# Kernel tuning notes

Hardware: AMD Instinct MI355X
Metric: run time of the kernel (lower is better)

The kernel has to match this reference:

```python
import jax, jax.numpy as jnp
import numpy as np

NUM_PER_PATH = 16
MARGIN_INTRA = 0.1
MARGIN_INTER = 1.0


def setup_inputs() -> dict:
    key = jax.random.key(0)
    # [B, block_num, 1, 1, 2]; trailing dims must multiply to 2 (see _get_center view)
    path_fea = jax.random.normal(key, (131072, 64, 1, 1, 2), dtype=jnp.float32)
    return {"path_fea": path_fea}


def reference(path_fea):
    B, block = path_fea.shape[0], path_fea.shape[1]
    D = block * 2                     # flattened per-sample feature dim
    G = B // NUM_PER_PATH             # number of centers (groups)
    fea = path_fea.reshape(B, D)      # [B, D] (matches path_fea[j].view(-1))

    # center: mean over the NUM_PER_PATH samples of each group, per block
    # (identical math to the permute/view dance in _get_center)
    grouped = fea.reshape(G, NUM_PER_PATH, D)          # [G, P, D]
    center = jnp.mean(grouped, axis=1)                 # [G, D]

    # ---- inter loss: hinge on pairwise euclidean distances between centers ----
    sq = jnp.sum(center * center, axis=1)              # [G]
    gram = center @ center.T                           # [G, G]
    d2 = jnp.maximum(sq[:, None] + sq[None, :] - 2.0 * gram, 0.0)
    pair_mask = jnp.triu(jnp.ones((G, G), dtype=bool), k=1)  # i < j
    d = jnp.sqrt(jnp.where(pair_mask, d2, 1.0))        # safe sqrt off-mask
    hinge = jnp.maximum(MARGIN_INTER - d, 0.0) ** 2
    n_pairs = G * (G - 1) / 2.0
    inter_loss = jnp.sum(jnp.where(pair_mask, hinge, 0.0)) / n_pairs

    # ---- intra loss: hinge on distance of each sample to its group center ----
    diff = grouped - center[:, None, :]                # [G, P, D]
    di = jnp.sqrt(jnp.sum(diff * diff, axis=-1))       # [G, P]
    intra_loss = jnp.sum(jnp.maximum(di - MARGIN_INTRA, 0.0) ** 2) / (G * NUM_PER_PATH)

    return (inter_loss, intra_loss)
```

## Files before the change

kernel.cpp:

```cpp
#include <hip/hip_runtime.h>
#include <hip/hip_bf16.h>
#include <math.h>

#define B_ROWS   131072
#define D_DIM    128
#define P_SAMP   16
#define G_GROUPS 8192
#define T128     64
#define NTRI2    2080
#define K1_BLOCKS (G_GROUPS / 4)

typedef __bf16 bf16x8  __attribute__((ext_vector_type(8)));
typedef float  floatx4 __attribute__((ext_vector_type(4)));
typedef unsigned short u16x8 __attribute__((ext_vector_type(8)));


__device__ __forceinline__ float wave_red64(float v) {
    #pragma unroll
    for (int off = 32; off > 0; off >>= 1) v += __shfl_xor(v, off, 64);
    return v;
}

__global__ __launch_bounds__(256) void k_center_intra(
    const float* __restrict__ x,
    uint2* __restrict__ cfrag,
    float* __restrict__ sq,
    float* __restrict__ partial,
    float* __restrict__ acc)
{
    const int wave = threadIdx.x >> 6;
    const int lane = threadIdx.x & 63;
    const int half = lane >> 5;
    const int c    = lane & 31;
    const int g    = blockIdx.x * 4 + wave;

    if (blockIdx.x == 0 && threadIdx.x == 0) acc[0] = 0.f;

    const float* base = x + (size_t)g * (P_SAMP * D_DIM) + half * D_DIM + c * 4;

    floatx4 v[8];
    #pragma unroll
    for (int l = 0; l < 8; ++l)
        v[l] = *(const floatx4*)(base + l * (2 * D_DIM));

    floatx4 cs = v[0];
    #pragma unroll
    for (int l = 1; l < 8; ++l) cs += v[l];
    #pragma unroll
    for (int k = 0; k < 4; ++k) cs[k] += __shfl_xor(cs[k], 32, 64);
    floatx4 ctr = cs * (1.0f / P_SAMP);

    float p[9];
    #pragma unroll
    for (int l = 0; l < 8; ++l) {
        floatx4 d = v[l] - ctr;
        p[l] = d[0]*d[0] + d[1]*d[1] + d[2]*d[2] + d[3]*d[3];
    }
    p[8] = ctr[0]*ctr[0] + ctr[1]*ctr[1] + ctr[2]*ctr[2] + ctr[3]*ctr[3];

    #pragma unroll
    for (int off = 16; off > 0; off >>= 1) {
        #pragma unroll
        for (int s = 0; s < 9; ++s) p[s] += __shfl_xor(p[s], off, 64);
    }

    if (half == 0) {
        unsigned int b0 = __builtin_bit_cast(unsigned short, (__bf16)ctr[0]);
        unsigned int b1 = __builtin_bit_cast(unsigned short, (__bf16)ctr[1]);
        unsigned int b2 = __builtin_bit_cast(unsigned short, (__bf16)ctr[2]);
        unsigned int b3 = __builtin_bit_cast(unsigned short, (__bf16)ctr[3]);
        uint2 pk;
        pk.x = (b1 << 16) | b0;
        pk.y = (b3 << 16) | b2;
        const int gran = (g >> 4) * 256 + (c >> 1) * 16 + (g & 15);
        cfrag[gran * 2 + (c & 1)] = pk;
    }
    if (lane == 0) sq[g] = p[8];

    float isum = 0.f;
    #pragma unroll
    for (int l = 0; l < 8; ++l) {
        float d = sqrtf(p[l]);
        float t = fmaxf(d - 0.1f, 0.f);
        isum += t * t;
    }
    isum += __shfl_xor(isum, 32, 64);

    __shared__ float sh[4];
    if (lane == 0) sh[wave] = isum;
    __syncthreads();
    if (threadIdx.x == 0)
        partial[blockIdx.x] = sh[0] + sh[1] + sh[2] + sh[3];
}

__global__ __launch_bounds__(256) void k_inter(
    const u16x8* __restrict__ cfrag,
    const float* __restrict__ sq,
    float* __restrict__ acc)
{
    __shared__ u16x8 smem[4096];

    const int bid = blockIdx.x;
    float sf = sqrtf(64.5f * 64.5f - 2.0f * (float)bid);
    int ti = (int)(64.5f - sf);
    if (ti < 0) ti = 0;
    if (ti > T128 - 1) ti = T128 - 1;
    #define TRI_OFF(i) ((i) * T128 - (((i) * ((i) - 1)) >> 1))
    while (ti > 0 && TRI_OFF(ti) > bid) --ti;
    while (ti < T128 - 1 && TRI_OFF(ti + 1) <= bid) ++ti;
    const int tj = ti + (bid - TRI_OFF(ti));
    #undef TRI_OFF

    const int t = threadIdx.x;
    const size_t abase = (size_t)ti * 2048;
    const size_t bbase = (size_t)tj * 2048;
    #pragma unroll
    for (int it = 0; it < 8; ++it) {
        const int idx = t + it * 256;
        smem[idx]        = cfrag[abase + idx];
        smem[idx + 2048] = cfrag[bbase + idx];
    }
    __syncthreads();

    const int wave = t >> 6;
    const int lane = t & 63;
    const int wr   = wave >> 1;
    const int wc   = wave & 1;
    const int lrow = lane & 15;
    const int quad = lane >> 4;

    const bool bdiag = (ti == tj);
    if (bdiag && wr > wc) return;

    const int i0 = ti * 128 + wr * 64;
    const int j0 = tj * 128 + wc * 64;

    floatx4 sqi[4];
    float   sqj[4];
    #pragma unroll
    for (int mt = 0; mt < 4; ++mt)
        sqi[mt] = *(const floatx4*)(sq + i0 + mt * 16 + quad * 4);
    #pragma unroll
    for (int nt = 0; nt < 4; ++nt)
        sqj[nt] = sq[j0 + nt * 16 + lrow];

    floatx4 c4[4][4] = {};

    #pragma unroll
    for (int ks = 0; ks < 4; ++ks) {
        const int go = (ks * 4 + quad) * 16 + lrow;
        bf16x8 a[4], b[4];
        #pragma unroll
        for (int mt = 0; mt < 4; ++mt)
            a[mt] = __builtin_bit_cast(bf16x8, smem[(wr * 4 + mt) * 256 + go]);
        #pragma unroll
        for (int nt = 0; nt < 4; ++nt)
            b[nt] = __builtin_bit_cast(bf16x8, smem[2048 + (wc * 4 + nt) * 256 + go]);
        #pragma unroll
        for (int mt = 0; mt < 4; ++mt)
            #pragma unroll
            for (int nt = 0; nt < 4; ++nt)
                c4[mt][nt] = __builtin_amdgcn_mfma_f32_16x16x32_bf16(
                                a[mt], b[nt], c4[mt][nt], 0, 0, 0);
    }

    const bool qdiag = (bdiag && wr == wc);
    float hsum = 0.f;
    #pragma unroll
    for (int mt = 0; mt < 4; ++mt) {
        #pragma unroll
        for (int nt = 0; nt < 4; ++nt) {
            const int ib = i0 + mt * 16 + quad * 4;
            const int j  = j0 + nt * 16 + lrow;
            #pragma unroll
            for (int r = 0; r < 4; ++r) {
                if (qdiag && j <= ib + r) continue;
                float d2 = sqi[mt][r] + sqj[nt] - 2.0f * c4[mt][nt][r];
                if (d2 < 1.0f) {
                    float d = sqrtf(fmaxf(d2, 0.f));
                    float tt = 1.0f - d;
                    hsum += tt * tt;
                }
            }
        }
    }
    if (__ballot(hsum != 0.f)) {
        hsum = wave_red64(hsum);
        if (lane == 0) atomicAdd(acc, hsum);
    }
}

__global__ __launch_bounds__(256) void k_final(
    const float* __restrict__ acc,
    const float* __restrict__ partial,
    float* __restrict__ out)
{
    __shared__ float sh[4];
    float s = 0.f;
    for (int i = threadIdx.x; i < K1_BLOCKS; i += 256) s += partial[i];
    s = wave_red64(s);
    const int wave = threadIdx.x >> 6;
    const int lane = threadIdx.x & 63;
    if (lane == 0) sh[wave] = s;
    __syncthreads();
    if (threadIdx.x == 0) {
        const float n_pairs = (float)G_GROUPS * (float)(G_GROUPS - 1) * 0.5f;
        out[0] = acc[0] / n_pairs;
        out[1] = (sh[0] + sh[1] + sh[2] + sh[3]) / (float)B_ROWS;
    }
}

extern "C" void kernel_launch(void* const* d_in, const int* in_sizes, int n_in,
                              void* d_out, int out_size, void* d_ws, size_t ws_size,
                              hipStream_t stream) {
    const float* x = (const float*)d_in[0];
    float* out = (float*)d_out;

    float* acc     = (float*)d_ws;
    float* partial = (float*)((char*)d_ws + 256);
    float* sq      = (float*)((char*)d_ws + 16384);
    uint2* cfrag   = (uint2*)((char*)d_ws + 65536);

    k_center_intra<<<K1_BLOCKS, 256, 0, stream>>>(x, cfrag, sq, partial, acc);

    k_inter<<<NTRI2, 256, 0, stream>>>((const u16x8*)cfrag, sq, acc);

    k_final<<<1, 256, 0, stream>>>(acc, partial, out);
}
```

Before: 120.3 us.

## Process chunks of four column tiles per block, loading B fragments from global

Each block of the inter-center kernel now keeps one row tile of centers in shared memory and loops over up to four column tiles. The column tile's bf16 fragments are read directly from global memory into registers, with the next k-slice prefetched while the current one is multiplied. The intent is to reuse the A tile across several tiles, cut the block count and the per-block LDS fill cost, and reduce atomic adds. Launch bounds now request 3 blocks per CU. The trade-off is fewer blocks (544) with uneven work along the triangle, global-load latency in the inner loop, and a serial loop to map each block to its tile chunk.

```diff
diff --git a/kernel.cpp b/kernel.cpp
--- a/kernel.cpp
+++ b/kernel.cpp
@@ -7,7 +7,8 @@
 #define P_SAMP   16
 #define G_GROUPS 8192
 #define T128     64
-#define NTRI2    2080
+#define CHUNK    4
+#define NCHUNK   544
 #define K1_BLOCKS (G_GROUPS / 4)
 
 typedef __bf16 bf16x8  __attribute__((ext_vector_type(8)));
@@ -93,33 +94,29 @@
         partial[blockIdx.x] = sh[0] + sh[1] + sh[2] + sh[3];
 }
 
-__global__ __launch_bounds__(256) void k_inter(
+__global__ __launch_bounds__(256, 3) void k_inter(
     const u16x8* __restrict__ cfrag,
     const float* __restrict__ sq,
     float* __restrict__ acc)
 {
-    __shared__ u16x8 smem[4096];
-
-    const int bid = blockIdx.x;
-    float sf = sqrtf(64.5f * 64.5f - 2.0f * (float)bid);
-    int ti = (int)(64.5f - sf);
-    if (ti < 0) ti = 0;
-    if (ti > T128 - 1) ti = T128 - 1;
-    #define TRI_OFF(i) ((i) * T128 - (((i) * ((i) - 1)) >> 1))
-    while (ti > 0 && TRI_OFF(ti) > bid) --ti;
-    while (ti < T128 - 1 && TRI_OFF(ti + 1) <= bid) ++ti;
-    const int tj = ti + (bid - TRI_OFF(ti));
-    #undef TRI_OFF
+    __shared__ u16x8 smemA[2048];
+
+    int rem = blockIdx.x;
+    int ti = 0;
+    for (;;) {
+        int n = (T128 - ti + CHUNK - 1) / CHUNK;
+        if (rem < n) break;
+        rem -= n;
+        ++ti;
+    }
+    const int tj0   = ti + rem * CHUNK;
+    const int tjend = min(tj0 + CHUNK, T128);
 
     const int t = threadIdx.x;
     const size_t abase = (size_t)ti * 2048;
-    const size_t bbase = (size_t)tj * 2048;
-    #pragma unroll
-    for (int it = 0; it < 8; ++it) {
-        const int idx = t + it * 256;
-        smem[idx]        = cfrag[abase + idx];
-        smem[idx + 2048] = cfrag[bbase + idx];
-    }
+    #pragma unroll
+    for (int it = 0; it < 8; ++it)
+        smemA[t + it * 256] = cfrag[abase + t + it * 256];
     __syncthreads();
 
     const int wave = t >> 6;
@@ -129,61 +126,80 @@
     const int lrow = lane & 15;
     const int quad = lane >> 4;
 
-    const bool bdiag = (ti == tj);
-    if (bdiag && wr > wc) return;
-
     const int i0 = ti * 128 + wr * 64;
-    const int j0 = tj * 128 + wc * 64;
 
     floatx4 sqi[4];
-    float   sqj[4];
     #pragma unroll
     for (int mt = 0; mt < 4; ++mt)
         sqi[mt] = *(const floatx4*)(sq + i0 + mt * 16 + quad * 4);
-    #pragma unroll
-    for (int nt = 0; nt < 4; ++nt)
-        sqj[nt] = sq[j0 + nt * 16 + lrow];
-
-    floatx4 c4[4][4] = {};
-
-    #pragma unroll
-    for (int ks = 0; ks < 4; ++ks) {
-        const int go = (ks * 4 + quad) * 16 + lrow;
-        bf16x8 a[4], b[4];
-        #pragma unroll
-        for (int mt = 0; mt < 4; ++mt)
-            a[mt] = __builtin_bit_cast(bf16x8, smem[(wr * 4 + mt) * 256 + go]);
+
+    float hsum = 0.f;
+
+    for (int tj = tj0; tj < tjend; ++tj) {
+        const bool bdiag = (tj == ti);
+        if (bdiag && wr > wc) continue;
+
+        const int j0 = tj * 128 + wc * 64;
+
+        float sqj[4];
         #pragma unroll
         for (int nt = 0; nt < 4; ++nt)
-            b[nt] = __builtin_bit_cast(bf16x8, smem[2048 + (wc * 4 + nt) * 256 + go]);
-        #pragma unroll
-        for (int mt = 0; mt < 4; ++mt)
+            sqj[nt] = sq[j0 + nt * 16 + lrow];
+
+        #define BIDX(nt, ks) (((size_t)tj * 8 + wc * 4 + (nt)) * 256 + ((ks) * 4 + quad) * 16 + lrow)
+
+        bf16x8 bb[2][4];
+        #pragma unroll
+        for (int pb = 0; pb < 2; ++pb)
             #pragma unroll
             for (int nt = 0; nt < 4; ++nt)
-                c4[mt][nt] = __builtin_amdgcn_mfma_f32_16x16x32_bf16(
-                                a[mt], b[nt], c4[mt][nt], 0, 0, 0);
-    }
-
-    const bool qdiag = (bdiag && wr == wc);
-    float hsum = 0.f;
-    #pragma unroll
-    for (int mt = 0; mt < 4; ++mt) {
-        #pragma unroll
-        for (int nt = 0; nt < 4; ++nt) {
-            const int ib = i0 + mt * 16 + quad * 4;
-            const int j  = j0 + nt * 16 + lrow;
-            #pragma unroll
-            for (int r = 0; r < 4; ++r) {
-                if (qdiag && j <= ib + r) continue;
-                float d2 = sqi[mt][r] + sqj[nt] - 2.0f * c4[mt][nt][r];
-                if (d2 < 1.0f) {
-                    float d = sqrtf(fmaxf(d2, 0.f));
-                    float tt = 1.0f - d;
-                    hsum += tt * tt;
+                bb[pb][nt] = __builtin_bit_cast(bf16x8, cfrag[BIDX(nt, pb)]);
+
+        floatx4 c4[4][4] = {};
+
+        #pragma unroll
+        for (int ks = 0; ks < 4; ++ks) {
+            const int cur = ks & 1;
+            bf16x8 a[4];
+            const int go = (ks * 4 + quad) * 16 + lrow;
+            #pragma unroll
+            for (int mt = 0; mt < 4; ++mt)
+                a[mt] = __builtin_bit_cast(bf16x8, smemA[(wr * 4 + mt) * 256 + go]);
+            #pragma unroll
+            for (int mt = 0; mt < 4; ++mt)
+                #pragma unroll
+                for (int nt = 0; nt < 4; ++nt)
+                    c4[mt][nt] = __builtin_amdgcn_mfma_f32_16x16x32_bf16(
+                                    a[mt], bb[cur][nt], c4[mt][nt], 0, 0, 0);
+            if (ks < 2) {
+                #pragma unroll
+                for (int nt = 0; nt < 4; ++nt)
+                    bb[cur][nt] = __builtin_bit_cast(bf16x8, cfrag[BIDX(nt, ks + 2)]);
+            }
+        }
+        #undef BIDX
+
+        const bool qdiag = (bdiag && wr == wc);
+        #pragma unroll
+        for (int mt = 0; mt < 4; ++mt) {
+            #pragma unroll
+            for (int nt = 0; nt < 4; ++nt) {
+                const int ib = i0 + mt * 16 + quad * 4;
+                const int j  = j0 + nt * 16 + lrow;
+                #pragma unroll
+                for (int r = 0; r < 4; ++r) {
+                    if (qdiag && j <= ib + r) continue;
+                    float d2 = sqi[mt][r] + sqj[nt] - 2.0f * c4[mt][nt][r];
+                    if (d2 < 1.0f) {
+                        float d = sqrtf(fmaxf(d2, 0.f));
+                        float tt = 1.0f - d;
+                        hsum += tt * tt;
+                    }
                 }
             }
         }
     }
+
     if (__ballot(hsum != 0.f)) {
         hsum = wave_red64(hsum);
         if (lane == 0) atomicAdd(acc, hsum);
@@ -223,7 +239,7 @@
 
     k_center_intra<<<K1_BLOCKS, 256, 0, stream>>>(x, cfrag, sq, partial, acc);
 
-    k_inter<<<NTRI2, 256, 0, stream>>>((const u16x8*)cfrag, sq, acc);
+    k_inter<<<NCHUNK, 256, 0, stream>>>((const u16x8*)cfrag, sq, acc);
 
     k_final<<<1, 256, 0, stream>>>(acc, partial, out);
 }
```

Result: faster. 117.5 us (-2.3%).
